# Optimization experiments

Measured on AMD Instinct MI355X. Metric: run time of the kernel, lower is better.

The kernel has to match this reference:

```python
import jax, jax.numpy as jnp
import numpy as np

EPS = 1e-7  # K.epsilon()


def setup_inputs() -> dict:
    key = jax.random.key(0)
    k1, k2 = jax.random.split(key)
    B, m, n = 4096, 256, 256
    y = jax.random.normal(k1, (B, n), dtype=jnp.float32)
    A = jax.random.normal(k2, (m, n), dtype=jnp.float32)
    b = jnp.ones((m,), dtype=jnp.float32)   # Ac = 0 < b, so c is interior
    c = jnp.zeros((n,), dtype=jnp.float32)
    return {"y": y, "A": A, "b": b, "c": c}


def reference(y, A, b, c):
    # Ac and residual b - Ac  -> [m]
    Ac = A @ c
    b_minus_Ac = b - Ac
    # A (y - c): broadcast-matmul expressed as einsum  -> [B, m]
    y_minus_c = y - c
    A_dot = jnp.einsum("mn,bn->bm", A, y_minus_c)
    # candidate intersection scalars along the line y->c
    ip = b_minus_Ac / (A_dot + EPS)
    cand = jnp.where(ip > 1.0, 2.0, ip)
    cand = jnp.where(cand < 0.0, 2.0, cand)
    alpha = jnp.min(cand, axis=-1, keepdims=True)      # [B, 1]
    alpha = jnp.where(alpha > 1.0, 1.0, alpha)          # interior point -> keep y
    z = alpha * y + (1.0 - alpha) * c
    return z
```

## Files before the change

### kernel.cpp

```cpp
#include <hip/hip_runtime.h>
#include <hip/hip_bf16.h>

#define EPS 1e-7f
#define LDSW 260

typedef __attribute__((ext_vector_type(8))) short short8;
typedef __attribute__((ext_vector_type(4))) float f32x4;

__device__ __forceinline__ unsigned pk(float a, float b) {
    __hip_bfloat162 h2 = __float22bfloat162_rn(make_float2(a, b));
    unsigned r; __builtin_memcpy(&r, &h2, 4); return r;
}

__device__ __forceinline__ short8 mk8(float4 f0, float4 f1) {
    uint4 u;
    u.x = pk(f0.x, f0.y); u.y = pk(f0.z, f0.w);
    u.z = pk(f1.x, f1.y); u.w = pk(f1.z, f1.w);
    short8 r; __builtin_memcpy(&r, &u, 16); return r;
}

__global__ __launch_bounds__(512, 1)
void fused_kernel(const float* __restrict__ y, const float* __restrict__ A,
                  const float* __restrict__ bb, const float* __restrict__ c,
                  float* __restrict__ z)
{
    __shared__ float ymc[16][LDSW];
    __shared__ float red[8][16];
    __shared__ float alphas[16];

    const int t    = threadIdx.x;
    const int w    = t >> 6;
    const int lane = t & 63;
    const int lr   = lane & 15;
    const int lg   = lane >> 4;
    const int b0   = blockIdx.x * 16;

    const float4* y4  = (const float4*)y;
    const float4* c4g = (const float4*)c;
    float4* z4 = (float4*)z;

    #pragma unroll
    for (int k = 0; k < 2; ++k) {
        int pos = t + k * 512;
        int row = pos >> 6, col4 = pos & 63;
        float4 yv = y4[(size_t)(b0 + row) * 64 + col4];
        float4 cv = c4g[col4];
        float4 r;
        r.x = yv.x - cv.x; r.y = yv.y - cv.y;
        r.z = yv.z - cv.z; r.w = yv.w - cv.w;
        *(float4*)&ymc[row][col4 * 4] = r;
    }
    __syncthreads();

    f32x4 acc0  = {0.f,0.f,0.f,0.f};
    f32x4 acc1  = {0.f,0.f,0.f,0.f};
    f32x4 accc0 = {0.f,0.f,0.f,0.f};
    f32x4 accc1 = {0.f,0.f,0.f,0.f};

    const int MT0 = 2 * w, MT1 = MT0 + 1;
    const float* a0 = A + (size_t)(MT0 * 16 + lr) * 256;
    const float* a1 = A + (size_t)(MT1 * 16 + lr) * 256;

    #pragma unroll
    for (int s = 0; s < 8; ++s) {
        const int col = 32 * s + 8 * lg;
        float4 yv0 = *(const float4*)&ymc[lr][col];
        float4 yv1 = *(const float4*)&ymc[lr][col + 4];
        short8 af = mk8(yv0, yv1);
        float4 a00 = *(const float4*)(a0 + col);
        float4 a01 = *(const float4*)(a0 + col + 4);
        float4 a10 = *(const float4*)(a1 + col);
        float4 a11 = *(const float4*)(a1 + col + 4);
        short8 bf0 = mk8(a00, a01);
        short8 bf1 = mk8(a10, a11);
        float4 cv0 = *(const float4*)(c + col);
        float4 cv1 = *(const float4*)(c + col + 4);
        short8 cf = mk8(cv0, cv1);

        acc0  = __builtin_amdgcn_mfma_f32_16x16x32_bf16(af, bf0, acc0,  0, 0, 0);
        acc1  = __builtin_amdgcn_mfma_f32_16x16x32_bf16(af, bf1, acc1,  0, 0, 0);
        accc0 = __builtin_amdgcn_mfma_f32_16x16x32_bf16(cf, bf0, accc0, 0, 0, 0);
        accc1 = __builtin_amdgcn_mfma_f32_16x16x32_bf16(cf, bf1, accc1, 0, 0, 0);
    }

    const int m0 = MT0 * 16 + lr;
    const int m1 = MT1 * 16 + lr;
    const float bm0 = bb[m0] - accc0[0];
    const float bm1 = bb[m1] - accc1[0];

    float cmin[4];
    #pragma unroll
    for (int q = 0; q < 4; ++q) {
        float ip0 = bm0 / (acc0[q] + EPS);
        float ip1 = bm1 / (acc1[q] + EPS);
        float c0 = (ip0 > 1.f || ip0 < 0.f) ? 2.f : ip0;
        float c1 = (ip1 > 1.f || ip1 < 0.f) ? 2.f : ip1;
        cmin[q] = fminf(c0, c1);
    }
    #pragma unroll
    for (int q = 0; q < 4; ++q) {
        float v = cmin[q];
        v = fminf(v, __shfl_xor(v, 1));
        v = fminf(v, __shfl_xor(v, 2));
        v = fminf(v, __shfl_xor(v, 4));
        v = fminf(v, __shfl_xor(v, 8));
        cmin[q] = v;
    }
    if (lr == 0) {
        #pragma unroll
        for (int q = 0; q < 4; ++q) red[w][lg * 4 + q] = cmin[q];
    }
    __syncthreads();

    if (t < 16) {
        float a = red[0][t];
        #pragma unroll
        for (int i = 1; i < 8; ++i) a = fminf(a, red[i][t]);
        alphas[t] = fminf(a, 1.0f);
    }
    __syncthreads();

    #pragma unroll
    for (int k = 0; k < 2; ++k) {
        int pos = t + k * 512;
        int row = pos >> 6, col4 = pos & 63;
        float al = alphas[row];
        float4 m  = *(const float4*)&ymc[row][col4 * 4];
        float4 cv = c4g[col4];
        float4 o;
        o.x = fmaf(al, m.x, cv.x);
        o.y = fmaf(al, m.y, cv.y);
        o.z = fmaf(al, m.z, cv.z);
        o.w = fmaf(al, m.w, cv.w);
        z4[(size_t)(b0 + row) * 64 + col4] = o;
    }
}

extern "C" void kernel_launch(void* const* d_in, const int* in_sizes, int n_in,
                              void* d_out, int out_size, void* d_ws, size_t ws_size,
                              hipStream_t stream) {
    const float* y = (const float*)d_in[0];
    const float* A = (const float*)d_in[1];
    const float* b = (const float*)d_in[2];
    const float* c = (const float*)d_in[3];
    float* z = (float*)d_out;

    const int B = in_sizes[0] / 256;
    fused_kernel<<<B / 16, 512, 0, stream>>>(y, A, b, c, z);
}
```

Baseline: 70.40 us.

## Use 1024-thread blocks with one m-tile per wave and prefetched A fragments

Doubles the block to 16 waves so each wave handles a single 16-row tile of A instead of two, halving the MFMA chain per wave. It also hoists A loads and the bf16 conversion into registers before the barrier so they overlap the y staging, and keeps c in registers for the final store. The aim is more latency hiding and parallelism per block, at the cost of more waves, a larger reduction array, and higher register pressure under the new launch bounds.

```diff
diff --git a/kernel.cpp b/kernel.cpp
--- a/kernel.cpp
+++ b/kernel.cpp
@@ -19,13 +19,13 @@
     short8 r; __builtin_memcpy(&r, &u, 16); return r;
 }
 
-__global__ __launch_bounds__(512, 1)
+__global__ __launch_bounds__(1024, 4)
 void fused_kernel(const float* __restrict__ y, const float* __restrict__ A,
                   const float* __restrict__ bb, const float* __restrict__ c,
                   float* __restrict__ z)
 {
     __shared__ float ymc[16][LDSW];
-    __shared__ float red[8][16];
+    __shared__ float red[16][16];
     __shared__ float alphas[16];
 
     const int t    = threadIdx.x;
@@ -39,63 +39,47 @@
     const float4* c4g = (const float4*)c;
     float4* z4 = (float4*)z;
 
+    const int row  = t >> 6;
+    const int col4 = t & 63;
+    float4 yv  = y4[(size_t)(b0 + row) * 64 + col4];
+    float4 cvs = c4g[col4];
+
+    const float* arow = A + (size_t)(w * 16 + lr) * 256;
+    short8 bf[8];
     #pragma unroll
-    for (int k = 0; k < 2; ++k) {
-        int pos = t + k * 512;
-        int row = pos >> 6, col4 = pos & 63;
-        float4 yv = y4[(size_t)(b0 + row) * 64 + col4];
-        float4 cv = c4g[col4];
-        float4 r;
-        r.x = yv.x - cv.x; r.y = yv.y - cv.y;
-        r.z = yv.z - cv.z; r.w = yv.w - cv.w;
-        *(float4*)&ymc[row][col4 * 4] = r;
+    for (int s = 0; s < 8; ++s) {
+        const float4* ap = (const float4*)(arow + 32 * s + 8 * lg);
+        bf[s] = mk8(ap[0], ap[1]);
     }
+    const float bmb = bb[w * 16 + lr];
+
+    float4 r;
+    r.x = yv.x - cvs.x; r.y = yv.y - cvs.y;
+    r.z = yv.z - cvs.z; r.w = yv.w - cvs.w;
+    *(float4*)&ymc[row][col4 * 4] = r;
     __syncthreads();
 
-    f32x4 acc0  = {0.f,0.f,0.f,0.f};
-    f32x4 acc1  = {0.f,0.f,0.f,0.f};
-    f32x4 accc0 = {0.f,0.f,0.f,0.f};
-    f32x4 accc1 = {0.f,0.f,0.f,0.f};
-
-    const int MT0 = 2 * w, MT1 = MT0 + 1;
-    const float* a0 = A + (size_t)(MT0 * 16 + lr) * 256;
-    const float* a1 = A + (size_t)(MT1 * 16 + lr) * 256;
-
+    f32x4 acc  = {0.f, 0.f, 0.f, 0.f};
+    f32x4 accc = {0.f, 0.f, 0.f, 0.f};
     #pragma unroll
     for (int s = 0; s < 8; ++s) {
         const int col = 32 * s + 8 * lg;
         float4 yv0 = *(const float4*)&ymc[lr][col];
         float4 yv1 = *(const float4*)&ymc[lr][col + 4];
         short8 af = mk8(yv0, yv1);
-        float4 a00 = *(const float4*)(a0 + col);
-        float4 a01 = *(const float4*)(a0 + col + 4);
-        float4 a10 = *(const float4*)(a1 + col);
-        float4 a11 = *(const float4*)(a1 + col + 4);
-        short8 bf0 = mk8(a00, a01);
-        short8 bf1 = mk8(a10, a11);
         float4 cv0 = *(const float4*)(c + col);
         float4 cv1 = *(const float4*)(c + col + 4);
         short8 cf = mk8(cv0, cv1);
-
-        acc0  = __builtin_amdgcn_mfma_f32_16x16x32_bf16(af, bf0, acc0,  0, 0, 0);
-        acc1  = __builtin_amdgcn_mfma_f32_16x16x32_bf16(af, bf1, acc1,  0, 0, 0);
-        accc0 = __builtin_amdgcn_mfma_f32_16x16x32_bf16(cf, bf0, accc0, 0, 0, 0);
-        accc1 = __builtin_amdgcn_mfma_f32_16x16x32_bf16(cf, bf1, accc1, 0, 0, 0);
+        acc  = __builtin_amdgcn_mfma_f32_16x16x32_bf16(af, bf[s], acc,  0, 0, 0);
+        accc = __builtin_amdgcn_mfma_f32_16x16x32_bf16(cf, bf[s], accc, 0, 0, 0);
     }
 
-    const int m0 = MT0 * 16 + lr;
-    const int m1 = MT1 * 16 + lr;
-    const float bm0 = bb[m0] - accc0[0];
-    const float bm1 = bb[m1] - accc1[0];
-
+    const float bm = bmb - accc[0];
     float cmin[4];
     #pragma unroll
     for (int q = 0; q < 4; ++q) {
-        float ip0 = bm0 / (acc0[q] + EPS);
-        float ip1 = bm1 / (acc1[q] + EPS);
-        float c0 = (ip0 > 1.f || ip0 < 0.f) ? 2.f : ip0;
-        float c1 = (ip1 > 1.f || ip1 < 0.f) ? 2.f : ip1;
-        cmin[q] = fminf(c0, c1);
+        float ip = bm / (acc[q] + EPS);
+        cmin[q] = (ip > 1.f || ip < 0.f) ? 2.f : ip;
     }
     #pragma unroll
     for (int q = 0; q < 4; ++q) {
@@ -115,23 +99,19 @@
     if (t < 16) {
         float a = red[0][t];
         #pragma unroll
-        for (int i = 1; i < 8; ++i) a = fminf(a, red[i][t]);
+        for (int i = 1; i < 16; ++i) a = fminf(a, red[i][t]);
         alphas[t] = fminf(a, 1.0f);
     }
     __syncthreads();
 
-    #pragma unroll
-    for (int k = 0; k < 2; ++k) {
-        int pos = t + k * 512;
-        int row = pos >> 6, col4 = pos & 63;
+    {
         float al = alphas[row];
         float4 m  = *(const float4*)&ymc[row][col4 * 4];
-        float4 cv = c4g[col4];
         float4 o;
-        o.x = fmaf(al, m.x, cv.x);
-        o.y = fmaf(al, m.y, cv.y);
-        o.z = fmaf(al, m.z, cv.z);
-        o.w = fmaf(al, m.w, cv.w);
+        o.x = fmaf(al, m.x, cvs.x);
+        o.y = fmaf(al, m.y, cvs.y);
+        o.z = fmaf(al, m.z, cvs.z);
+        o.w = fmaf(al, m.w, cvs.w);
         z4[(size_t)(b0 + row) * 64 + col4] = o;
     }
 }
@@ -146,5 +126,5 @@
     float* z = (float*)d_out;
 
     const int B = in_sizes[0] / 256;
-    fused_kernel<<<B / 16, 512, 0, stream>>>(y, A, b, c, z);
+    fused_kernel<<<B / 16, 1024, 0, stream>>>(y, A, b, c, z);
 }
```

New measurement: 71.01 us. Within noise of the previous version (+0.9%).

## Stage full bf16-converted A in LDS and read y directly from global

Applied to the files above, without the earlier changes.

Each block now loads all of A, converts it to bf16 in MFMA fragment order, and stores it in a 128KB LDS buffer before the MMA loop. The y rows are read straight from global memory instead. A(y-c) is now formed as Ay minus Ac, and the epilogue re-reads y from global. The aim is to remove the per-wave strided global reads of A, but it adds a large LDS footprint and a full barrier before any MFMA work. The 128KB LDS use also makes the launch-bounds hint of two blocks per CU unachievable.

```diff
diff --git a/kernel.cpp b/kernel.cpp
--- a/kernel.cpp
+++ b/kernel.cpp
@@ -2,7 +2,6 @@
 #include <hip/hip_bf16.h>
 
 #define EPS 1e-7f
-#define LDSW 260
 
 typedef __attribute__((ext_vector_type(8))) short short8;
 typedef __attribute__((ext_vector_type(4))) float f32x4;
@@ -19,36 +18,31 @@
     short8 r; __builtin_memcpy(&r, &u, 16); return r;
 }
 
-__global__ __launch_bounds__(512, 1)
+__global__ __launch_bounds__(512, 2)
 void fused_kernel(const float* __restrict__ y, const float* __restrict__ A,
                   const float* __restrict__ bb, const float* __restrict__ c,
                   float* __restrict__ z)
 {
-    __shared__ float ymc[16][LDSW];
+    __shared__ short8 Asw[8192];
     __shared__ float red[8][16];
     __shared__ float alphas[16];
 
     const int t    = threadIdx.x;
+    const int lane = t & 63;
     const int w    = t >> 6;
-    const int lane = t & 63;
     const int lr   = lane & 15;
     const int lg   = lane >> 4;
     const int b0   = blockIdx.x * 16;
 
-    const float4* y4  = (const float4*)y;
-    const float4* c4g = (const float4*)c;
-    float4* z4 = (float4*)z;
-
     #pragma unroll
-    for (int k = 0; k < 2; ++k) {
-        int pos = t + k * 512;
-        int row = pos >> 6, col4 = pos & 63;
-        float4 yv = y4[(size_t)(b0 + row) * 64 + col4];
-        float4 cv = c4g[col4];
-        float4 r;
-        r.x = yv.x - cv.x; r.y = yv.y - cv.y;
-        r.z = yv.z - cv.z; r.w = yv.w - cv.w;
-        *(float4*)&ymc[row][col4 * 4] = r;
+    for (int k = 0; k < 16; ++k) {
+        const int u = t + 512 * k;
+        const int l = u & 63;
+        const int s = (u >> 6) & 7;
+        const int T = u >> 9;
+        const float4* ap =
+            (const float4*)(A + (size_t)(16 * T + (l & 15)) * 256 + 32 * s + 8 * (l >> 4));
+        Asw[u] = mk8(ap[0], ap[1]);
     }
     __syncthreads();
 
@@ -58,25 +52,18 @@
     f32x4 accc1 = {0.f,0.f,0.f,0.f};
 
     const int MT0 = 2 * w, MT1 = MT0 + 1;
-    const float* a0 = A + (size_t)(MT0 * 16 + lr) * 256;
-    const float* a1 = A + (size_t)(MT1 * 16 + lr) * 256;
+    const float4* yp = (const float4*)(y + (size_t)(b0 + lr) * 256) + lg * 2;
 
     #pragma unroll
     for (int s = 0; s < 8; ++s) {
-        const int col = 32 * s + 8 * lg;
-        float4 yv0 = *(const float4*)&ymc[lr][col];
-        float4 yv1 = *(const float4*)&ymc[lr][col + 4];
-        short8 af = mk8(yv0, yv1);
-        float4 a00 = *(const float4*)(a0 + col);
-        float4 a01 = *(const float4*)(a0 + col + 4);
-        float4 a10 = *(const float4*)(a1 + col);
-        float4 a11 = *(const float4*)(a1 + col + 4);
-        short8 bf0 = mk8(a00, a01);
-        short8 bf1 = mk8(a10, a11);
-        float4 cv0 = *(const float4*)(c + col);
-        float4 cv1 = *(const float4*)(c + col + 4);
+        float4 f0 = yp[8 * s];
+        float4 f1 = yp[8 * s + 1];
+        short8 af = mk8(f0, f1);
+        float4 cv0 = *(const float4*)(c + 32 * s + 8 * lg);
+        float4 cv1 = *(const float4*)(c + 32 * s + 8 * lg + 4);
         short8 cf = mk8(cv0, cv1);
-
+        short8 bf0 = Asw[(MT0 * 8 + s) * 64 + lane];
+        short8 bf1 = Asw[(MT1 * 8 + s) * 64 + lane];
         acc0  = __builtin_amdgcn_mfma_f32_16x16x32_bf16(af, bf0, acc0,  0, 0, 0);
         acc1  = __builtin_amdgcn_mfma_f32_16x16x32_bf16(af, bf1, acc1,  0, 0, 0);
         accc0 = __builtin_amdgcn_mfma_f32_16x16x32_bf16(cf, bf0, accc0, 0, 0, 0);
@@ -91,8 +78,10 @@
     float cmin[4];
     #pragma unroll
     for (int q = 0; q < 4; ++q) {
-        float ip0 = bm0 / (acc0[q] + EPS);
-        float ip1 = bm1 / (acc1[q] + EPS);
+        float d0 = acc0[q] - accc0[q];
+        float d1 = acc1[q] - accc1[q];
+        float ip0 = bm0 / (d0 + EPS);
+        float ip1 = bm1 / (d1 + EPS);
         float c0 = (ip0 > 1.f || ip0 < 0.f) ? 2.f : ip0;
         float c1 = (ip1 > 1.f || ip1 < 0.f) ? 2.f : ip1;
         cmin[q] = fminf(c0, c1);
@@ -120,18 +109,21 @@
     }
     __syncthreads();
 
+    const float4* y4  = (const float4*)y;
+    const float4* c4g = (const float4*)c;
+    float4* z4 = (float4*)z;
     #pragma unroll
     for (int k = 0; k < 2; ++k) {
         int pos = t + k * 512;
         int row = pos >> 6, col4 = pos & 63;
-        float al = alphas[row];
-        float4 m  = *(const float4*)&ymc[row][col4 * 4];
+        float al  = alphas[row];
+        float4 yv = y4[(size_t)(b0 + row) * 64 + col4];
         float4 cv = c4g[col4];
         float4 o;
-        o.x = fmaf(al, m.x, cv.x);
-        o.y = fmaf(al, m.y, cv.y);
-        o.z = fmaf(al, m.z, cv.z);
-        o.w = fmaf(al, m.w, cv.w);
+        o.x = fmaf(al, yv.x - cv.x, cv.x);
+        o.y = fmaf(al, yv.y - cv.y, cv.y);
+        o.z = fmaf(al, yv.z - cv.z, cv.z);
+        o.w = fmaf(al, yv.w - cv.w, cv.w);
         z4[(size_t)(b0 + row) * 64 + col4] = o;
     }
 }
```

Result: slower. 73.77 us (+4.8%).
